# Optimization experiments

Measured on AMD Instinct MI355X. Metric: run time of the kernel, lower is better.

## Reference

```python
import jax, jax.numpy as jnp
import numpy as np

D = 1024; DI = 2048; HS = 16; PS = DI // HS; NS = 64; KC = 4; CHUNK = 64
HA = 16; HKV = 4; PA = D // HA; MLP_MULT = 4; ROPE_BASE = 10000.0
B_SZ = 2; L_SEQ = 2048


def rms_norm(x):
    eps = jnp.asarray(jnp.finfo(x.dtype).eps, x.dtype)
    return x * jax.lax.rsqrt(jnp.mean(jnp.square(x), axis=-1, keepdims=True) + eps)


def silu(x):
    return x * jax.nn.sigmoid(x)


def apply_rope(x, cos, sin):
    half = x.shape[-1] // 2
    x1, x2 = x[..., :half], x[..., half:]
    return jnp.concatenate([x1 * cos + x2 * sin, -x1 * sin + x2 * cos], axis=-1)


def selective_scan(x, A, Bm, Cm, dt, chunk):
    # x: [B,L,H,P], Bm/Cm: [B,L,H,N], A/dt: [H]. L must be a multiple of chunk.
    Bb, L, H, P = x.shape
    N = Bm.shape[-1]
    decay = jnp.exp(A * dt)  # [H]
    nc = L // chunk
    xp = x.reshape(Bb, nc, chunk, H, P).transpose(0, 1, 3, 2, 4)   # [B,nc,H,cs,P]
    Bp = Bm.reshape(Bb, nc, chunk, H, N).transpose(0, 1, 3, 2, 4)  # [B,nc,H,cs,N]
    Cp = Cm.reshape(Bb, nc, chunk, H, N).transpose(0, 1, 3, 2, 4)
    x_dt = xp * dt[None, None, :, None, None]
    idx = jnp.arange(chunk)
    diff = idx[:, None] - idx[None, :]
    # intra-chunk causal decay matrix L_mat: [H,cs,cs]
    Lm = jnp.where(diff >= 0, decay[:, None, None] ** jnp.maximum(diff, 0), 0.0)
    CB = jnp.einsum('bchqn,bchkn->bchqk', Cp, Bp)
    y_diag = jnp.einsum('bchqk,bchkp->bchqp', CB * Lm[None, None], x_dt)
    # per-chunk states
    decay_rev = decay[:, None] ** (chunk - 1 - idx)[None, :]  # [H,cs]
    states = jnp.einsum('bchtn,bchtp->bchnp', Bp * decay_rev[None, None, :, :, None], x_dt)
    # inter-chunk propagation
    ci = jnp.arange(nc)
    shift = ci[:, None] - ci[None, :] - 1
    cdec = decay ** chunk
    M = jnp.where(shift >= 0, cdec[:, None, None] ** jnp.maximum(shift, 0), 0.0)  # [H,nc,nc]
    h_carry = jnp.einsum('hij,bjhnp->bihnp', M, states)
    decay_out = decay[:, None] ** (idx + 1)[None, :]  # [H,cs]
    y_off = jnp.einsum('bchtn,bchnp->bchtp', Cp, h_carry) * decay_out[None, None, :, :, None]
    y = (y_diag + y_off).transpose(0, 1, 3, 2, 4).reshape(Bb, L, H, P)
    return y


def mlp(n, fc_w, proj_w):
    h = jax.nn.relu(n @ fc_w)
    return jnp.square(h) @ proj_w


def setup_inputs() -> dict:
    key = jax.random.key(0)
    ks = jax.random.split(key, 24)
    w = lambda k, shp, s=0.02: jax.random.normal(k, shp, jnp.float32) * s
    dt_init = jax.random.uniform(ks[0], (HS,), jnp.float32, 0.001, 0.1)
    dt_bias = dt_init + jnp.log(-jnp.expm1(-dt_init))  # inverse softplus
    return {
        'x': jax.random.normal(ks[1], (B_SZ, L_SEQ, D), jnp.float32),
        'in_proj_w': w(ks[2], (D, 2 * DI)),
        'conv_w': w(ks[3], (DI, KC), 0.2),
        'conv_b': jnp.zeros((DI,), jnp.float32),
        'B_proj_w': w(ks[4], (D, HS * NS)),
        'C_proj_w': w(ks[5], (D, HS * NS)),
        'dt_bias': dt_bias,
        'A_log': jnp.log(jnp.arange(1, HS + 1, dtype=jnp.float32)),
        'D_param': jnp.ones((HS,), jnp.float32),
        'out_proj_w': w(ks[6], (DI, D)),
        'resid_mix_m': jnp.stack([jnp.ones(D), jnp.zeros(D)]).astype(jnp.float32),
        'mamba_scale': jnp.ones((D,), jnp.float32),
        'm_fc_w': w(ks[7], (D, MLP_MULT * D)),
        'm_proj_w': w(ks[8], (MLP_MULT * D, D)),
        'm_mlp_scale': jnp.ones((D,), jnp.float32),
        'resid_mix_a': jnp.stack([jnp.ones(D), jnp.zeros(D)]).astype(jnp.float32),
        'q_w': w(ks[9], (D, D)),
        'k_w': w(ks[10], (D, HKV * PA)),
        'v_w': w(ks[11], (D, HKV * PA)),
        'o_w': w(ks[12], (D, D)),
        'q_gain': jnp.full((HA,), 1.0, jnp.float32),
        'attn_scale': jnp.ones((D,), jnp.float32),
        'a_fc_w': w(ks[13], (D, MLP_MULT * D)),
        'a_proj_w': w(ks[14], (MLP_MULT * D, D)),
        'a_mlp_scale': jnp.ones((D,), jnp.float32),
    }


def reference(x, in_proj_w, conv_w, conv_b, B_proj_w, C_proj_w, dt_bias, A_log, D_param, out_proj_w, resid_mix_m, mamba_scale, m_fc_w, m_proj_w, m_mlp_scale, resid_mix_a, q_w, k_w, v_w, o_w, q_gain, attn_scale, a_fc_w, a_proj_w, a_mlp_scale):
    Bb, L, _ = x.shape
    x0 = x
    # ---- Mamba block ----
    xm = resid_mix_m[0][None, None] * x + resid_mix_m[1][None, None] * x0
    n = rms_norm(xm)
    vg = n @ in_proj_w
    value, gate = vg[..., :DI], vg[..., DI:]
    v_t = value.transpose(0, 2, 1)  # [B, DI, L]
    v_conv = jax.lax.conv_general_dilated(
        v_t, conv_w[:, None, :], (1,), [(KC - 1, 0)],
        feature_group_count=DI, dimension_numbers=('NCH', 'OIH', 'NCH')) + conv_b[None, :, None]
    value = silu(v_conv).transpose(0, 2, 1).reshape(Bb, L, HS, PS)
    Bm = (xm @ B_proj_w).reshape(Bb, L, HS, NS)  # B/C use pre-norm (mixed) input
    Cm = (xm @ C_proj_w).reshape(Bb, L, HS, NS)
    dt = jax.nn.softplus(dt_bias)
    A = -jnp.exp(A_log)
    y = selective_scan(value, A, Bm, Cm, dt, CHUNK)
    y = y + D_param[None, None, :, None] * value
    y = (y.reshape(Bb, L, DI) * silu(gate)) @ out_proj_w
    xm = xm + mamba_scale[None, None] * y
    xm = xm + m_mlp_scale[None, None] * mlp(rms_norm(xm), m_fc_w, m_proj_w)
    # ---- Attention block ----
    xa = resid_mix_a[0][None, None] * xm + resid_mix_a[1][None, None] * x0
    n = rms_norm(xa)
    q = (n @ q_w).reshape(Bb, L, HA, PA).transpose(0, 2, 1, 3)
    k = (n @ k_w).reshape(Bb, L, HKV, PA).transpose(0, 2, 1, 3)
    v = (n @ v_w).reshape(Bb, L, HKV, PA).transpose(0, 2, 1, 3)
    q = rms_norm(q); k = rms_norm(k)
    inv_freq = 1.0 / (ROPE_BASE ** (jnp.arange(0, PA, 2, dtype=jnp.float32) / PA))
    f = jnp.outer(jnp.arange(L, dtype=jnp.float32), inv_freq)
    cos, sin = jnp.cos(f)[None, None], jnp.sin(f)[None, None]
    q = apply_rope(q, cos, sin) * q_gain[None, :, None, None]
    k = apply_rope(k, cos, sin)
    G = HA // HKV
    k = jnp.repeat(k, G, axis=1); v = jnp.repeat(v, G, axis=1)
    s = jnp.einsum('bhqd,bhkd->bhqk', q, k) / np.float32(np.sqrt(PA))
    mask = jnp.tril(jnp.ones((L, L), bool))
    s = jnp.where(mask[None, None], s, jnp.asarray(-jnp.inf, s.dtype))
    att = jax.nn.softmax(s, axis=-1)
    y = jnp.einsum('bhqk,bhkd->bhqd', att, v).transpose(0, 2, 1, 3).reshape(Bb, L, D)
    xa = xa + attn_scale[None, None] * (y @ o_w)
    xa = xa + a_mlp_scale[None, None] * mlp(rms_norm(xa), a_fc_w, a_proj_w)
    return xa
```

## Files before the change

kernel.cpp:

```cpp
#include <hip/hip_runtime.h>
#include <hip/hip_bf16.h>
#include <math.h>

#define D_ 1024
#define DI_ 2048
#define HS_ 16
#define PS_ 128
#define NS_ 64
#define HA_ 16
#define HKV_ 4
#define PA_ 64
#define B_ 2
#define L_ 2048
#define NT_ 4096
#define NC_ 32
#define RMS_EPS_ 1.1920929e-7f

typedef __attribute__((ext_vector_type(8))) short short8;
typedef __attribute__((ext_vector_type(4))) float f32x4;

#define GLOAD_LDS16(gp, lp)                                                        \
  __builtin_amdgcn_global_load_lds(                                               \
      (const __attribute__((address_space(1))) unsigned int*)(gp),                \
      (__attribute__((address_space(3))) unsigned int*)(lp), 16, 0, 0)

__global__ __launch_bounds__(256) void transpose_cvt(
    const float* __restrict__ W, __hip_bfloat16* __restrict__ Wt, int K, int N, int ldw) {
  __shared__ float t[32][33];
  int n0 = blockIdx.x * 32, k0 = blockIdx.y * 32;
  int tx = threadIdx.x & 31, ty = threadIdx.x >> 5;
#pragma unroll
  for (int i = 0; i < 4; i++)
    t[ty + i * 8][tx] = W[(size_t)(k0 + ty + i * 8) * ldw + n0 + tx];
  __syncthreads();
#pragma unroll
  for (int i = 0; i < 4; i++)
    Wt[(size_t)(n0 + ty + i * 8) * K + k0 + tx] = __float2bfloat16(t[tx][ty + i * 8]);
}

template<int MODE>
__global__ __launch_bounds__(512) void gemm256_k32(
    const unsigned short* __restrict__ A, const unsigned short* __restrict__ Wt,
    __hip_bfloat16* __restrict__ Cb, int N, int K) {
  __shared__ unsigned short As[3][256 * 32];
  __shared__ unsigned short Bs[3][256 * 32];
  int lid = blockIdx.x;
  int x = lid & 7, r = lid >> 3;
  int bm = ((x >> 2) * 8 + (r & 7)) * 256;
  int bn = ((x & 3) * 4 + (r >> 3)) * 256;
  int tid = threadIdx.x;
  int w = tid >> 6, l = tid & 63;
  int wr = w >> 2, wc = w & 3;
  int l15 = l & 15, lg = l >> 4;
  int rr = tid >> 2, ss = tid & 3;

  f32x4 acc[8][4];
#pragma unroll
  for (int i = 0; i < 8; i++)
#pragma unroll
    for (int j = 0; j < 4; j++) acc[i][j] = (f32x4){0.f, 0.f, 0.f, 0.f};

  auto STAGE = [&](int kt, int nb) {
    int k0 = kt * 32;
#pragma unroll
    for (int p = 0; p < 2; p++) {
      int row = p * 128 + rr;
      int kq = ss ^ ((row >> 1) & 3);
      GLOAD_LDS16(A + (size_t)(bm + row) * K + k0 + kq * 8, &As[nb][row * 32 + ss * 8]);
    }
#pragma unroll
    for (int p = 0; p < 2; p++) {
      int row = p * 128 + rr;
      int kq = ss ^ ((row >> 1) & 3);
      GLOAD_LDS16(Wt + (size_t)(bn + row) * K + k0 + kq * 8, &Bs[nb][row * 32 + ss * 8]);
    }
  };

  int KT = K >> 5;
  STAGE(0, 0);
  STAGE(1, 1);
  int buf = 0;
  for (int t = 0; t < KT; ++t) {
    if (t + 1 < KT) {
      asm volatile("s_waitcnt vmcnt(4)" ::: "memory");
    } else {
      asm volatile("s_waitcnt vmcnt(0)" ::: "memory");
    }
    __builtin_amdgcn_s_barrier();
    __builtin_amdgcn_sched_barrier(0);
    if (t + 2 < KT) STAGE(t + 2, (t + 2) % 3);
    short8 bf[4];
#pragma unroll
    for (int j = 0; j < 4; j++) {
      int row = wc * 64 + j * 16 + l15;
      bf[j] = *(const short8*)&Bs[buf][row * 32 + ((lg ^ ((row >> 1) & 3)) << 3)];
    }
#pragma unroll
    for (int i = 0; i < 8; i++) {
      int row = wr * 128 + i * 16 + l15;
      short8 af = *(const short8*)&As[buf][row * 32 + ((lg ^ ((row >> 1) & 3)) << 3)];
#pragma unroll
      for (int j = 0; j < 4; j++)
        acc[i][j] = __builtin_amdgcn_mfma_f32_16x16x32_bf16(af, bf[j], acc[i][j], 0, 0, 0);
    }
    buf = (buf == 2) ? 0 : buf + 1;
  }
#pragma unroll
  for (int i = 0; i < 8; i++)
#pragma unroll
    for (int j = 0; j < 4; j++) {
      int gr = bm + wr * 128 + i * 16 + lg * 4;
      int gc = bn + wc * 64 + j * 16 + l15;
#pragma unroll
      for (int reg = 0; reg < 4; reg++) {
        float v = acc[i][j][reg];
        if (MODE == 1) { v = fmaxf(v, 0.f); v = v * v; }
        Cb[(size_t)(gr + reg) * N + gc] = __float2bfloat16(v);
      }
    }
}

template<int BN>
__global__ __launch_bounds__(256) void gemm_bf16_t(
    const unsigned short* __restrict__ A, const unsigned short* __restrict__ Wt,
    float* __restrict__ Cf, __hip_bfloat16* __restrict__ Cb,
    const float* __restrict__ baseb, const float* __restrict__ scale,
    int N, int K, int gn, int mode, int rsh) {
  constexpr int nWc = BN / 64;
  constexpr int nWr = 4 / nWc;
  constexpr int MF  = 8 / nWr;
  __shared__ unsigned short As[2][128 * 64];
  __shared__ unsigned short Bs[2][BN * 64];
  int lid = blockIdx.x;
  int x = lid & 7, r = lid >> 3;
  int bm, bn;
  if (rsh == 0) {
    int RN = gn >> 2;
    bm = ((x >> 2) * 16 + (r & 15)) * 128;
    bn = ((x & 3) * RN + (r >> 4)) * BN;
  } else {
    bm = (x * 4 + (r & 3)) * 128;
    bn = (r >> 2) * BN;
  }
  int tid = threadIdx.x;
  int w = tid >> 6, l = tid & 63;
  int wr = w / nWc, wc = w % nWc;
  int l15 = l & 15, lg = l >> 4;
  f32x4 acc[MF][4];
#pragma unroll
  for (int i = 0; i < MF; i++)
#pragma unroll
    for (int j = 0; j < 4; j++) acc[i][j] = (f32x4){0.f, 0.f, 0.f, 0.f};
  int r_ = tid >> 3;
  int s_ = tid & 7;

  auto STAGE = [&](int k0, int nb) {
#pragma unroll
    for (int i = 0; i < 4; i++) {
      int rr = i * 32 + r_;
      int kq = s_ ^ (rr & 7);
      GLOAD_LDS16(A + (size_t)(bm + rr) * K + k0 + kq * 8, &As[nb][rr * 64 + s_ * 8]);
    }
#pragma unroll
    for (int i = 0; i < BN / 32; i++) {
      int rr = i * 32 + r_;
      int kq = s_ ^ (rr & 7);
      GLOAD_LDS16(Wt + (size_t)(bn + rr) * K + k0 + kq * 8, &Bs[nb][rr * 64 + s_ * 8]);
    }
  };

  STAGE(0, 0);
  __syncthreads();
  int cur = 0;
  for (int k0 = 0; k0 < K; k0 += 64) {
    if (k0 + 64 < K) STAGE(k0 + 64, cur ^ 1);
#pragma unroll
    for (int h = 0; h < 2; h++) {
      short8 af[MF], bfr[4];
#pragma unroll
      for (int i = 0; i < MF; i++) {
        int row = wr * (16 * MF) + i * 16 + l15;
        int c = h * 4 + lg;
        af[i] = *(const short8*)&As[cur][row * 64 + ((c ^ (row & 7)) << 3)];
      }
#pragma unroll
      for (int j = 0; j < 4; j++) {
        int row = wc * 64 + j * 16 + l15;
        int c = h * 4 + lg;
        bfr[j] = *(const short8*)&Bs[cur][row * 64 + ((c ^ (row & 7)) << 3)];
      }
#pragma unroll
      for (int i = 0; i < MF; i++)
#pragma unroll
        for (int j = 0; j < 4; j++)
          acc[i][j] = __builtin_amdgcn_mfma_f32_16x16x32_bf16(af[i], bfr[j], acc[i][j], 0, 0, 0);
    }
    __syncthreads();
    cur ^= 1;
  }
  int rb = lg * 4, cb2 = l15;
#pragma unroll
  for (int i = 0; i < MF; i++)
#pragma unroll
    for (int j = 0; j < 4; j++) {
      int gr = bm + wr * (16 * MF) + i * 16 + rb;
      int gc = bn + wc * 64 + j * 16 + cb2;
#pragma unroll
      for (int reg = 0; reg < 4; reg++) {
        float v = acc[i][j][reg];
        size_t idx = (size_t)(gr + reg) * N + gc;
        if (mode == 0) {
          Cf[idx] = v;
        } else if (mode == 1) {
          v = fmaxf(v, 0.f);
          Cb[idx] = __float2bfloat16(v * v);
        } else if (mode == 2) {
          Cb[idx] = __float2bfloat16(v);
        } else {
          Cf[idx] = baseb[idx] + scale[gc] * v;
        }
      }
    }
}

__global__ __launch_bounds__(256) void mix_rms_kernel(
    const float* __restrict__ a, const float* __restrict__ b2,
    const float* __restrict__ mix, float* __restrict__ xout,
    __hip_bfloat16* __restrict__ nbf, __hip_bfloat16* __restrict__ rawbf) {
  int row = blockIdx.x;
  size_t base = (size_t)row * D_;
  float v[4]; float ss = 0.f;
#pragma unroll
  for (int i = 0; i < 4; i++) {
    int d = threadIdx.x + i * 256;
    float val = mix[d] * a[base + d] + mix[D_ + d] * b2[base + d];
    v[i] = val; ss += val * val;
  }
  for (int o = 32; o > 0; o >>= 1) ss += __shfl_down(ss, o, 64);
  __shared__ float red[4];
  if ((threadIdx.x & 63) == 0) red[threadIdx.x >> 6] = ss;
  __syncthreads();
  float inv = rsqrtf((red[0] + red[1] + red[2] + red[3]) * (1.f / D_) + RMS_EPS_);
#pragma unroll
  for (int i = 0; i < 4; i++) {
    int d = threadIdx.x + i * 256;
    xout[base + d] = v[i];
    nbf[base + d] = __float2bfloat16(v[i] * inv);
    if (rawbf) rawbf[base + d] = __float2bfloat16(v[i]);
  }
}

__global__ __launch_bounds__(256) void rms_kernel(
    const float* __restrict__ a, __hip_bfloat16* __restrict__ nbf) {
  int row = blockIdx.x;
  size_t base = (size_t)row * D_;
  float v[4]; float ss = 0.f;
#pragma unroll
  for (int i = 0; i < 4; i++) {
    int d = threadIdx.x + i * 256;
    float val = a[base + d];
    v[i] = val; ss += val * val;
  }
  for (int o = 32; o > 0; o >>= 1) ss += __shfl_down(ss, o, 64);
  __shared__ float red[4];
  if ((threadIdx.x & 63) == 0) red[threadIdx.x >> 6] = ss;
  __syncthreads();
  float inv = rsqrtf((red[0] + red[1] + red[2] + red[3]) * (1.f / D_) + RMS_EPS_);
#pragma unroll
  for (int i = 0; i < 4; i++) {
    int d = threadIdx.x + i * 256;
    nbf[base + d] = __float2bfloat16(v[i] * inv);
  }
}

__global__ __launch_bounds__(256) void conv_silu_kernel(
    const __hip_bfloat16* __restrict__ vg, const float* __restrict__ cw,
    const float* __restrict__ cb, float* __restrict__ xv) {
  int idx = blockIdx.x * 256 + threadIdx.x;
  int c = idx & (DI_ - 1);
  int bl = idx >> 11;
  int l = bl & (L_ - 1);
  float acc = cb[c];
  float w0 = cw[c * 4 + 0], w1 = cw[c * 4 + 1], w2 = cw[c * 4 + 2], w3 = cw[c * 4 + 3];
  size_t rb = (size_t)bl * 4096 + c;
  if (l >= 3) acc += __bfloat162float(vg[rb - (size_t)3 * 4096]) * w0;
  if (l >= 2) acc += __bfloat162float(vg[rb - (size_t)2 * 4096]) * w1;
  if (l >= 1) acc += __bfloat162float(vg[rb - (size_t)1 * 4096]) * w2;
  acc += __bfloat162float(vg[rb]) * w3;
  xv[idx] = acc / (1.f + __expf(-acc));
}

__global__ __launch_bounds__(256) void scanA1_kernel(
    const float* __restrict__ xv, const __hip_bfloat16* __restrict__ BCm,
    const float* __restrict__ dt_bias, const float* __restrict__ A_log,
    float* __restrict__ st) {
  __shared__ __align__(16) float sm[4096 + 8192];
  float* Bs = sm;
  float* Xs = sm + 4096;
  int blk = blockIdx.x;
  int c = blk & 31, h = (blk >> 5) & 15, b = blk >> 9;
  float dt = log1pf(__expf(dt_bias[h]));
  float adt = -__expf(A_log[h]) * dt;
  int tid = threadIdx.x;
  int l0 = c * 64;
  size_t rB = ((size_t)(b * L_ + l0)) * 2048 + h * NS_;
#pragma unroll
  for (int i = 0; i < 16; i++) {
    int e = tid + i * 256;
    int t = e >> 6, n = e & 63;
    Bs[t * 64 + n] = __bfloat162float(BCm[rB + (size_t)t * 2048 + n]);
  }
  size_t rX = ((size_t)(b * L_ + l0)) * DI_ + h * PS_;
#pragma unroll
  for (int i = 0; i < 32; i++) {
    int e = tid + i * 256;
    int t = e >> 7, p = e & 127;
    Xs[t * 128 + p] = xv[rX + (size_t)t * DI_ + p];
  }
  __syncthreads();
  int pg = tid & 31;
  int ng = (tid >> 5) << 3;
  float acc[8][4];
#pragma unroll
  for (int nn = 0; nn < 8; nn++)
#pragma unroll
    for (int i = 0; i < 4; i++) acc[nn][i] = 0.f;
  for (int t = 0; t < 64; t++) {
    float dr = __expf(adt * (float)(63 - t));
    float4 x4 = *(const float4*)&Xs[t * 128 + pg * 4];
    float xd0 = x4.x * dr, xd1 = x4.y * dr, xd2 = x4.z * dr, xd3 = x4.w * dr;
#pragma unroll
    for (int nn = 0; nn < 8; nn++) {
      float bv = Bs[t * 64 + ng + nn];
      acc[nn][0] += bv * xd0; acc[nn][1] += bv * xd1;
      acc[nn][2] += bv * xd2; acc[nn][3] += bv * xd3;
    }
  }
  size_t sb = ((size_t)((b * HS_ + h) * NC_ + c)) * (NS_ * PS_);
#pragma unroll
  for (int nn = 0; nn < 8; nn++) {
    *(float4*)&st[sb + (size_t)(ng + nn) * PS_ + pg * 4] =
        make_float4(acc[nn][0] * dt, acc[nn][1] * dt, acc[nn][2] * dt, acc[nn][3] * dt);
  }
}

__global__ __launch_bounds__(256) void scanA2_kernel(
    const float* __restrict__ xv, const __hip_bfloat16* __restrict__ BCm,
    const float* __restrict__ dt_bias,
    const float* __restrict__ A_log, const float* __restrict__ D_param,
    float* __restrict__ y) {
  __shared__ __align__(16) float sm[4160 + 8192];
  float* Cb = sm;
  float* Bs = sm + 4160;
  float* Xs = sm + 4160;
  int blk = blockIdx.x;
  int c = blk & 31, h = (blk >> 5) & 15, b = blk >> 9;
  float dt = log1pf(__expf(dt_bias[h]));
  float adt = -__expf(A_log[h]) * dt;
  float Dp = D_param[h];
  int tid = threadIdx.x;
  int l0 = c * 64;
  size_t rB = ((size_t)(b * L_ + l0)) * 2048 + h * NS_;
#pragma unroll
  for (int i = 0; i < 16; i++) {
    int e = tid + i * 256;
    int t = e >> 6, n = e & 63;
    Bs[t * 64 + n] = __bfloat162float(BCm[rB + (size_t)t * 2048 + n]);
    Cb[t * 65 + n] = __bfloat162float(BCm[rB + 1024 + (size_t)t * 2048 + n]);
  }
  __syncthreads();
  int q = tid >> 2;
  int kb = (tid & 3) << 4;
  float cbl[16];
#pragma unroll
  for (int kk = 0; kk < 16; kk++) {
    int k = kb + kk;
    float a = 0.f;
    if (k <= q) {
      for (int n = 0; n < 64; n++) a += Cb[q * 65 + n] * Bs[k * 64 + n];
      a *= __expf(adt * (float)(q - k));
    }
    cbl[kk] = a;
  }
  __syncthreads();
#pragma unroll
  for (int kk = 0; kk < 16; kk++) Cb[q * 65 + kb + kk] = cbl[kk];
  size_t rX = ((size_t)(b * L_ + l0)) * DI_ + h * PS_;
#pragma unroll
  for (int i = 0; i < 32; i++) {
    int e = tid + i * 256;
    int t = e >> 7, p = e & 127;
    Xs[t * 128 + p] = xv[rX + (size_t)t * DI_ + p];
  }
  __syncthreads();
  int pg = tid & 31;
  int qg = (tid >> 5) << 3;
  float acc[8][4];
#pragma unroll
  for (int qq = 0; qq < 8; qq++)
#pragma unroll
    for (int i = 0; i < 4; i++) acc[qq][i] = 0.f;
  for (int k = 0; k < 64; k++) {
    float4 x4 = *(const float4*)&Xs[k * 128 + pg * 4];
#pragma unroll
    for (int qq = 0; qq < 8; qq++) {
      float s = Cb[(qg + qq) * 65 + k];
      acc[qq][0] += s * x4.x; acc[qq][1] += s * x4.y;
      acc[qq][2] += s * x4.z; acc[qq][3] += s * x4.w;
    }
  }
#pragma unroll
  for (int qq = 0; qq < 8; qq++) {
    int qr = qg + qq;
    float4 xq = *(const float4*)&Xs[qr * 128 + pg * 4];
    size_t yo = ((size_t)(b * L_ + l0 + qr)) * DI_ + h * PS_ + pg * 4;
    *(float4*)&y[yo] = make_float4(acc[qq][0] * dt + Dp * xq.x,
                                   acc[qq][1] * dt + Dp * xq.y,
                                   acc[qq][2] * dt + Dp * xq.z,
                                   acc[qq][3] * dt + Dp * xq.w);
  }
}

__global__ __launch_bounds__(256) void scanB1_kernel(
    float* __restrict__ st, const float* __restrict__ dt_bias,
    const float* __restrict__ A_log) {
  int slice = blockIdx.x & 3;
  int h = (blockIdx.x >> 2) & 15, b = blockIdx.x >> 6;
  float dt = log1pf(__expf(dt_bias[h]));
  float adt = -__expf(A_log[h]) * dt;
  float cdec = __expf(adt * 64.f);
  size_t base = ((size_t)(b * HS_ + h)) * NC_ * (NS_ * PS_) + slice * 2048 + threadIdx.x;
  float hreg[8];
#pragma unroll
  for (int j = 0; j < 8; j++) hreg[j] = 0.f;
  for (int c = 0; c < NC_; c++) {
    size_t o = base + (size_t)c * (NS_ * PS_);
#pragma unroll
    for (int j = 0; j < 8; j++) {
      float tmp = st[o + (size_t)j * 256];
      st[o + (size_t)j * 256] = hreg[j];
      hreg[j] = cdec * hreg[j] + tmp;
    }
  }
}

__global__ __launch_bounds__(256) void scanB2_kernel(
    const __hip_bfloat16* __restrict__ BCm, const float* __restrict__ st,
    const __hip_bfloat16* __restrict__ vg, const float* __restrict__ dt_bias,
    const float* __restrict__ A_log, const float* __restrict__ y,
    __hip_bfloat16* __restrict__ yout) {
  __shared__ float Cs[64 * 64];
  __shared__ __align__(16) float Hs[64 * 128];
  int blk = blockIdx.x;
  int c = blk & 31, h = (blk >> 5) & 15, b = blk >> 9;
  float dt = log1pf(__expf(dt_bias[h]));
  float adt = -__expf(A_log[h]) * dt;
  int tid = threadIdx.x;
  int l0 = c * 64;
  size_t rC = ((size_t)(b * L_ + l0)) * 2048 + 1024 + h * NS_;
#pragma unroll
  for (int i = 0; i < 16; i++) {
    int e = tid + i * 256;
    int t = e >> 6, n = e & 63;
    Cs[t * 64 + n] = __bfloat162float(BCm[rC + (size_t)t * 2048 + n]);
  }
  size_t sb = ((size_t)((b * HS_ + h) * NC_ + c)) * (NS_ * PS_);
#pragma unroll
  for (int i = 0; i < 32; i++) {
    int e = tid + i * 256;
    Hs[e] = st[sb + e];
  }
  __syncthreads();
  int pg = tid & 31;
  int tg = (tid >> 5) << 3;
  float acc[8][4];
#pragma unroll
  for (int tt = 0; tt < 8; tt++)
#pragma unroll
    for (int i = 0; i < 4; i++) acc[tt][i] = 0.f;
  for (int n = 0; n < 64; n++) {
    float4 h4 = *(const float4*)&Hs[n * 128 + pg * 4];
#pragma unroll
    for (int tt = 0; tt < 8; tt++) {
      float cv = Cs[(tg + tt) * 64 + n];
      acc[tt][0] += cv * h4.x; acc[tt][1] += cv * h4.y;
      acc[tt][2] += cv * h4.z; acc[tt][3] += cv * h4.w;
    }
  }
#pragma unroll
  for (int tt = 0; tt < 8; tt++) {
    int t = tg + tt;
    float dout = __expf(adt * (float)(t + 1));
    size_t row = (size_t)(b * L_ + l0 + t);
#pragma unroll
    for (int i = 0; i < 4; i++) {
      int p = pg * 4 + i;
      float g = __bfloat162float(vg[row * 4096 + 2048 + h * PS_ + p]);
      float yv = y[row * DI_ + h * PS_ + p] + acc[tt][i] * dout;
      yout[row * DI_ + h * PS_ + p] = __float2bfloat16(yv * (g / (1.f + __expf(-g))));
    }
  }
}

__global__ void rope_fill_kernel(float* __restrict__ cosb, float* __restrict__ sinb) {
  int idx = blockIdx.x * 256 + threadIdx.x;
  int i = idx & 31, l = idx >> 5;
  float inv = __expf(-(2.0f * (float)i / (float)PA_) * logf(10000.0f));
  float ang = (float)l * inv;
  cosb[idx] = cosf(ang);
  sinb[idx] = sinf(ang);
}

__global__ __launch_bounds__(256) void qknorm_rope_bf16_kernel(
    const float* __restrict__ src, int srcstride, int srcofs,
    __hip_bfloat16* __restrict__ dst, int nh,
    const float* __restrict__ cosb, const float* __restrict__ sinb,
    const float* __restrict__ gain) {
  int row = blockIdx.x * 4 + (threadIdx.x >> 6);
  int lane = threadIdx.x & 63;
  int h = row % nh;
  int tok = row / nh;
  int l = tok & (L_ - 1);
  float v = src[(size_t)tok * srcstride + srcofs + h * 64 + lane];
  float ss = v * v;
  for (int o = 32; o > 0; o >>= 1) ss += __shfl_xor(ss, o, 64);
  v *= rsqrtf(ss * (1.f / PA_) + RMS_EPS_);
  float partner = __shfl_xor(v, 32, 64);
  int i = lane & 31;
  float cth = cosb[l * 32 + i], sth = sinb[l * 32 + i];
  float out = (lane < 32) ? (v * cth + partner * sth) : (v * cth - partner * sth);
  if (gain) out *= gain[h];
  dst[(size_t)tok * (nh * 64) + h * 64 + lane] = __float2bfloat16(out);
}

__global__ __launch_bounds__(256) void attn_mfma_kernel(
    const unsigned short* __restrict__ qb, const unsigned short* __restrict__ kb,
    const unsigned short* __restrict__ vt, const float* __restrict__ qgain,
    __hip_bfloat16* __restrict__ ao) {
  __shared__ unsigned short Ks[64][72];
  __shared__ unsigned short Vs[64][72];
  __shared__ unsigned short Psm[4][16][72];
  int blk = blockIdx.x;
  int qi = blk & 15;
  int h  = (blk >> 4) & 15;
  int b  = blk >> 8;
  int hk = h >> 2;
  int tid = threadIdx.x;
  int w = tid >> 6, l = tid & 63;
  int l15 = l & 15, lg = l >> 4;
  int r0 = tid >> 3, s0 = tid & 7;
  float mstat = 8.0f * fabsf(qgain[h]);
  const unsigned short* kbase = kb + (size_t)b * L_ * (HKV_ * PA_) + hk * PA_ + s0 * 8;
  const unsigned short* vbase = vt + ((size_t)(b * HKV_ + hk) * PA_) * L_ + s0 * 8;

  for (int pass = 0; pass < 2; pass++) {
    int qt = pass ? (31 - qi) : qi;
    int q0 = qt * 64;
    int qw = q0 + w * 16;
    short8 qf[2];
    {
      size_t qrow = ((size_t)(b * L_ + qw + l15)) * (HA_ * PA_) + h * PA_;
      qf[0] = *(const short8*)&qb[qrow + lg * 8];
      qf[1] = *(const short8*)&qb[qrow + 32 + lg * 8];
    }
    f32x4 o_acc[4];
#pragma unroll
    for (int db = 0; db < 4; db++) o_acc[db] = (f32x4){0.f, 0.f, 0.f, 0.f};
    f32x4 lsum = (f32x4){0.f, 0.f, 0.f, 0.f};
    int nkt = qt + 1;
    short8 kr0 = *(const short8*)&kbase[(size_t)r0 * (HKV_ * PA_)];
    short8 kr1 = *(const short8*)&kbase[(size_t)(r0 + 32) * (HKV_ * PA_)];
    short8 vr0 = *(const short8*)&vbase[(size_t)r0 * L_];
    short8 vr1 = *(const short8*)&vbase[(size_t)(r0 + 32) * L_];
    for (int kt = 0; kt < nkt; kt++) {
      int k0 = kt * 64;
      __syncthreads();
      *(short8*)&Ks[r0][s0 * 8] = kr0;
      *(short8*)&Ks[r0 + 32][s0 * 8] = kr1;
      *(short8*)&Vs[r0][s0 * 8] = vr0;
      *(short8*)&Vs[r0 + 32][s0 * 8] = vr1;
      if (kt + 1 < nkt) {
        int k1 = k0 + 64;
        kr0 = *(const short8*)&kbase[(size_t)(k1 + r0) * (HKV_ * PA_)];
        kr1 = *(const short8*)&kbase[(size_t)(k1 + r0 + 32) * (HKV_ * PA_)];
        vr0 = *(const short8*)&vbase[(size_t)r0 * L_ + k1];
        vr1 = *(const short8*)&vbase[(size_t)(r0 + 32) * L_ + k1];
      }
      __syncthreads();
      f32x4 s_acc[4];
#pragma unroll
      for (int kb2 = 0; kb2 < 4; kb2++) {
        short8 b0 = *(const short8*)&Ks[kb2 * 16 + l15][lg * 8];
        short8 b1 = *(const short8*)&Ks[kb2 * 16 + l15][32 + lg * 8];
        f32x4 s = (f32x4){0.f, 0.f, 0.f, 0.f};
        s = __builtin_amdgcn_mfma_f32_16x16x32_bf16(qf[0], b0, s, 0, 0, 0);
        s = __builtin_amdgcn_mfma_f32_16x16x32_bf16(qf[1], b1, s, 0, 0, 0);
        s_acc[kb2] = s;
      }
      bool diag = (kt == qt);
#pragma unroll
      for (int kb2 = 0; kb2 < 4; kb2++) {
        int key = k0 + kb2 * 16 + l15;
#pragma unroll
        for (int reg = 0; reg < 4; reg++) {
          float p = __expf(s_acc[kb2][reg] * 0.125f - mstat);
          if (diag && key > qw + lg * 4 + reg) p = 0.f;
          lsum[reg] += p;
          __hip_bfloat16 hv = __float2bfloat16(p);
          Psm[w][lg * 4 + reg][kb2 * 16 + l15] = *(unsigned short*)&hv;
        }
      }
      asm volatile("s_waitcnt lgkmcnt(0)" ::: "memory");
#pragma unroll
      for (int ks = 0; ks < 2; ks++) {
        short8 pa = *(const short8*)&Psm[w][l15][ks * 32 + lg * 8];
#pragma unroll
        for (int db = 0; db < 4; db++) {
          short8 vb8 = *(const short8*)&Vs[db * 16 + l15][ks * 32 + lg * 8];
          o_acc[db] = __builtin_amdgcn_mfma_f32_16x16x32_bf16(pa, vb8, o_acc[db], 0, 0, 0);
        }
      }
    }
#pragma unroll
    for (int of = 1; of < 16; of <<= 1) {
      lsum[0] += __shfl_xor(lsum[0], of, 64);
      lsum[1] += __shfl_xor(lsum[1], of, 64);
      lsum[2] += __shfl_xor(lsum[2], of, 64);
      lsum[3] += __shfl_xor(lsum[3], of, 64);
    }
#pragma unroll
    for (int reg = 0; reg < 4; reg++) {
      float invl = 1.0f / lsum[reg];
      size_t row = (size_t)(b * L_ + qw + lg * 4 + reg);
#pragma unroll
      for (int db = 0; db < 4; db++)
        ao[row * D_ + h * PA_ + db * 16 + l15] = __float2bfloat16(o_acc[db][reg] * invl);
    }
  }
}

extern "C" void kernel_launch(void* const* d_in, const int* in_sizes, int n_in,
                              void* d_out, int out_size, void* d_ws, size_t ws_size,
                              hipStream_t stream) {
  (void)in_sizes; (void)n_in; (void)out_size; (void)ws_size;
  const float* x           = (const float*)d_in[0];
  const float* in_proj_w   = (const float*)d_in[1];
  const float* conv_w      = (const float*)d_in[2];
  const float* conv_b      = (const float*)d_in[3];
  const float* B_proj_w    = (const float*)d_in[4];
  const float* C_proj_w    = (const float*)d_in[5];
  const float* dt_bias     = (const float*)d_in[6];
  const float* A_log       = (const float*)d_in[7];
  const float* D_param     = (const float*)d_in[8];
  const float* out_proj_w  = (const float*)d_in[9];
  const float* resid_mix_m = (const float*)d_in[10];
  const float* mamba_scale = (const float*)d_in[11];
  const float* m_fc_w      = (const float*)d_in[12];
  const float* m_proj_w    = (const float*)d_in[13];
  const float* m_mlp_scale = (const float*)d_in[14];
  const float* resid_mix_a = (const float*)d_in[15];
  const float* q_w         = (const float*)d_in[16];
  const float* k_w         = (const float*)d_in[17];
  const float* v_w         = (const float*)d_in[18];
  const float* o_w         = (const float*)d_in[19];
  const float* q_gain      = (const float*)d_in[20];
  const float* attn_scale  = (const float*)d_in[21];
  const float* a_fc_w      = (const float*)d_in[22];
  const float* a_proj_w    = (const float*)d_in[23];
  const float* a_mlp_scale = (const float*)d_in[24];
  float* ws  = (float*)d_ws;
  float* out = (float*)d_out;

  float* xm    = ws;
  float* vgR   = ws + 4194304;
  float* xvR   = ws + 12582912;
  float* stR   = ws + 20971520;
  float* nbR   = ws + 29360128;
  float* xmbR  = ws + 31457280;
  float* BCR   = ws + 33554432;
  float* WtR   = ws + 37748736;
  float* cosb  = ws + 51642368;
  float* sinb  = cosb + 65536;

  __hip_bfloat16* vg  = (__hip_bfloat16*)vgR;
  float*          qkvf = vgR;
  float*          xv  = xvR;
  float*          st  = stR;
  __hip_bfloat16* hb  = (__hip_bfloat16*)stR;
  __hip_bfloat16* nbb = (__hip_bfloat16*)nbR;
  __hip_bfloat16* xmb = (__hip_bfloat16*)xmbR;
  __hip_bfloat16* ybb = (__hip_bfloat16*)nbR;
  __hip_bfloat16* BCm = (__hip_bfloat16*)BCR;
  __hip_bfloat16* qbb = (__hip_bfloat16*)xvR;
  __hip_bfloat16* kbb = (__hip_bfloat16*)(xvR + 2097152);
  __hip_bfloat16* vtb = (__hip_bfloat16*)(xvR + 2621440);
  __hip_bfloat16* aob = (__hip_bfloat16*)(xvR + 3145728);

  __hip_bfloat16* Wt = (__hip_bfloat16*)WtR;
  size_t o_in  = 0;
  size_t o_B   = o_in  + (size_t)4096 * 1024;
  size_t o_out = o_B   + (size_t)2048 * 1024;
  size_t o_mfc = o_out + (size_t)1024 * 2048;
  size_t o_mpj = o_mfc + (size_t)4096 * 1024;
  size_t o_qkv = o_mpj + (size_t)1024 * 4096;
  size_t o_o   = o_qkv + (size_t)1536 * 1024;
  size_t o_afc = o_o   + (size_t)1024 * 1024;
  size_t o_apj = o_afc + (size_t)4096 * 1024;

#define TCVT(Wp, off, K, N) \
  transpose_cvt<<<dim3((N) / 32, (K) / 32), 256, 0, stream>>>((Wp), Wt + (off), (K), (N), (N))
  TCVT(in_proj_w,  o_in,  1024, 4096);
  TCVT(B_proj_w,   o_B,   1024, 1024);
  TCVT(C_proj_w,   o_B + (size_t)1024 * 1024, 1024, 1024);
  TCVT(out_proj_w, o_out, 2048, 1024);
  TCVT(m_fc_w,     o_mfc, 1024, 4096);
  TCVT(m_proj_w,   o_mpj, 4096, 1024);
  TCVT(q_w,        o_qkv, 1024, 1024);
  TCVT(k_w,        o_qkv + (size_t)1024 * 1024, 1024, 256);
  TCVT(v_w,        o_qkv + (size_t)1280 * 1024, 1024, 256);
  TCVT(o_w,        o_o,   1024, 1024);
  TCVT(a_fc_w,     o_afc, 1024, 4096);
  TCVT(a_proj_w,   o_apj, 4096, 1024);
#undef TCVT

#define GEMM(BN, Abuf, Woff, Cfp, Cbp, basep, scalep, N, K, mode, rsh) \
  gemm_bf16_t<BN><<<32 * ((N) / (BN)), 256, 0, stream>>>( \
      (const unsigned short*)(Abuf), (const unsigned short*)(Wt + (Woff)), \
      (Cfp), (Cbp), (basep), (scalep), (N), (K), (N) / (BN), (mode), (rsh))
#define GEMM256(MODE, Abuf, Woff, Cbp) \
  gemm256_k32<MODE><<<256, 512, 0, stream>>>( \
      (const unsigned short*)(Abuf), (const unsigned short*)(Wt + (Woff)), \
      (Cbp), 4096, 1024)

  mix_rms_kernel<<<NT_, 256, 0, stream>>>(x, x, resid_mix_m, xm, nbb, xmb);
  GEMM256(2, nbb, o_in, vg);
  GEMM(128, xmb, o_B, (float*)0, BCm, (const float*)0, (const float*)0, 2048, 1024, 2, 0);
  conv_silu_kernel<<<NT_ * DI_ / 256, 256, 0, stream>>>(vg, conv_w, conv_b, xv);
  scanA1_kernel<<<B_ * HS_ * NC_, 256, 0, stream>>>(xv, BCm, dt_bias, A_log, st);
  scanA2_kernel<<<B_ * HS_ * NC_, 256, 0, stream>>>(xv, BCm, dt_bias, A_log, D_param, xv);
  scanB1_kernel<<<B_ * HS_ * 4, 256, 0, stream>>>(st, dt_bias, A_log);
  scanB2_kernel<<<B_ * HS_ * NC_, 256, 0, stream>>>(BCm, st, vg, dt_bias, A_log, xv, ybb);
  GEMM(64, ybb, o_out, xm, (__hip_bfloat16*)0, xm, mamba_scale, 1024, 2048, 3, 1);
  rms_kernel<<<NT_, 256, 0, stream>>>(xm, nbb);
  GEMM256(1, nbb, o_mfc, hb);
  GEMM(64, hb, o_mpj, xm, (__hip_bfloat16*)0, xm, m_mlp_scale, 1024, 4096, 3, 1);
  mix_rms_kernel<<<NT_, 256, 0, stream>>>(xm, x, resid_mix_a, xm, nbb, (__hip_bfloat16*)0);
  GEMM(64, nbb, o_qkv, qkvf, (__hip_bfloat16*)0, (const float*)0, (const float*)0, 1536, 1024, 0, 0);
  rope_fill_kernel<<<L_ * 32 / 256, 256, 0, stream>>>(cosb, sinb);
  qknorm_rope_bf16_kernel<<<NT_ * HA_ / 4, 256, 0, stream>>>(qkvf, 1536, 0, qbb, HA_, cosb, sinb, q_gain);
  qknorm_rope_bf16_kernel<<<NT_ * HKV_ / 4, 256, 0, stream>>>(qkvf, 1536, 1024, kbb, HKV_, cosb, sinb, (const float*)0);
  transpose_cvt<<<dim3(256 / 32, 2048 / 32), 256, 0, stream>>>(qkvf + 1280, vtb, 2048, 256, 1536);
  transpose_cvt<<<dim3(256 / 32, 2048 / 32), 256, 0, stream>>>(qkvf + (size_t)L_ * 1536 + 1280, vtb + (size_t)256 * L_, 2048, 256, 1536);
  attn_mfma_kernel<<<B_ * HA_ * 16, 256, 0, stream>>>(
      (const unsigned short*)qbb, (const unsigned short*)kbb, (const unsigned short*)vtb,
      q_gain, aob);
  GEMM(64, aob, o_o, xm, (__hip_bfloat16*)0, xm, attn_scale, 1024, 1024, 3, 0);
  rms_kernel<<<NT_, 256, 0, stream>>>(xm, nbb);
  GEMM256(1, nbb, o_afc, hb);
  GEMM(64, hb, o_apj, out, (__hip_bfloat16*)0, xm, a_mlp_scale, 1024, 4096, 3, 1);
#undef GEMM
#undef GEMM256
}
```

Before: 687.6 us.

## Add 64x64-tile double-buffered GEMM for narrow-N projections

Adds a new gemm64 kernel that uses 64x64 output tiles, double-buffered LDS staging through direct global-to-LDS loads with an XOR swizzle, and a grouped block-index mapping. It replaces the templated GEMM for the N=1024/1536 projections (out_proj, MLP down-projections, QKV, O). With 4096 rows the smaller tiles launch more blocks, which should fill the CUs better and overlap loads with MFMA work. The cost is less data reuse per block and more redundant reads of A and B.

```diff
diff --git a/kernel.cpp b/kernel.cpp
--- a/kernel.cpp
+++ b/kernel.cpp
@@ -221,6 +221,74 @@
         }
       }
     }
+}
+
+__global__ __launch_bounds__(256) void gemm64(
+    const unsigned short* __restrict__ A, const unsigned short* __restrict__ Wt,
+    float* __restrict__ Cf, const float* __restrict__ baseb,
+    const float* __restrict__ scale, int N, int K, int mode) {
+  __shared__ unsigned short As[2][64 * 64];
+  __shared__ unsigned short Bs[2][64 * 64];
+  int lid = blockIdx.x;
+  int x = lid & 7, r = lid >> 3;
+  int bm = (x * 8 + (r & 7)) * 64;
+  int bn = (r >> 3) * 64;
+  int tid = threadIdx.x;
+  int w = tid >> 6, l = tid & 63;
+  int l15 = l & 15, lg = l >> 4;
+  f32x4 acc[4];
+#pragma unroll
+  for (int j = 0; j < 4; j++) acc[j] = (f32x4){0.f, 0.f, 0.f, 0.f};
+  int r_ = tid >> 3;
+  int s_ = tid & 7;
+
+  auto STAGE = [&](int k0, int nb) {
+#pragma unroll
+    for (int i = 0; i < 2; i++) {
+      int row = i * 32 + r_;
+      int kq = s_ ^ (row & 7);
+      GLOAD_LDS16(A + (size_t)(bm + row) * K + k0 + kq * 8, &As[nb][row * 64 + s_ * 8]);
+    }
+#pragma unroll
+    for (int i = 0; i < 2; i++) {
+      int row = i * 32 + r_;
+      int kq = s_ ^ (row & 7);
+      GLOAD_LDS16(Wt + (size_t)(bn + row) * K + k0 + kq * 8, &Bs[nb][row * 64 + s_ * 8]);
+    }
+  };
+
+  STAGE(0, 0);
+  __syncthreads();
+  int cur = 0;
+  for (int k0 = 0; k0 < K; k0 += 64) {
+    if (k0 + 64 < K) STAGE(k0 + 64, cur ^ 1);
+#pragma unroll
+    for (int h = 0; h < 2; h++) {
+      int c = h * 4 + lg;
+      int arow = w * 16 + l15;
+      short8 af = *(const short8*)&As[cur][arow * 64 + ((c ^ (arow & 7)) << 3)];
+#pragma unroll
+      for (int j = 0; j < 4; j++) {
+        int brow = j * 16 + l15;
+        short8 bfr = *(const short8*)&Bs[cur][brow * 64 + ((c ^ (brow & 7)) << 3)];
+        acc[j] = __builtin_amdgcn_mfma_f32_16x16x32_bf16(af, bfr, acc[j], 0, 0, 0);
+      }
+    }
+    __syncthreads();
+    cur ^= 1;
+  }
+#pragma unroll
+  for (int j = 0; j < 4; j++) {
+    int gr = bm + w * 16 + lg * 4;
+    int gc = bn + j * 16 + l15;
+#pragma unroll
+    for (int reg = 0; reg < 4; reg++) {
+      float v = acc[j][reg];
+      size_t idx = (size_t)(gr + reg) * N + gc;
+      if (mode == 0) Cf[idx] = v;
+      else           Cf[idx] = baseb[idx] + scale[gc] * v;
+    }
+  }
 }
 
 __global__ __launch_bounds__(256) void mix_rms_kernel(
@@ -727,6 +795,10 @@
   gemm_bf16_t<BN><<<32 * ((N) / (BN)), 256, 0, stream>>>( \
       (const unsigned short*)(Abuf), (const unsigned short*)(Wt + (Woff)), \
       (Cfp), (Cbp), (basep), (scalep), (N), (K), (N) / (BN), (mode), (rsh))
+#define GEMM64(Abuf, Woff, Cfp, basep, scalep, N, K, mode) \
+  gemm64<<<64 * ((N) / 64), 256, 0, stream>>>( \
+      (const unsigned short*)(Abuf), (const unsigned short*)(Wt + (Woff)), \
+      (Cfp), (basep), (scalep), (N), (K), (mode))
 #define GEMM256(MODE, Abuf, Woff, Cbp) \
   gemm256_k32<MODE><<<256, 512, 0, stream>>>( \
       (const unsigned short*)(Abuf), (const unsigned short*)(Wt + (Woff)), \
@@ -740,12 +812,12 @@
   scanA2_kernel<<<B_ * HS_ * NC_, 256, 0, stream>>>(xv, BCm, dt_bias, A_log, D_param, xv);
   scanB1_kernel<<<B_ * HS_ * 4, 256, 0, stream>>>(st, dt_bias, A_log);
   scanB2_kernel<<<B_ * HS_ * NC_, 256, 0, stream>>>(BCm, st, vg, dt_bias, A_log, xv, ybb);
-  GEMM(64, ybb, o_out, xm, (__hip_bfloat16*)0, xm, mamba_scale, 1024, 2048, 3, 1);
+  GEMM64(ybb, o_out, xm, xm, mamba_scale, 1024, 2048, 3);
   rms_kernel<<<NT_, 256, 0, stream>>>(xm, nbb);
   GEMM256(1, nbb, o_mfc, hb);
-  GEMM(64, hb, o_mpj, xm, (__hip_bfloat16*)0, xm, m_mlp_scale, 1024, 4096, 3, 1);
+  GEMM64(hb, o_mpj, xm, xm, m_mlp_scale, 1024, 4096, 3);
   mix_rms_kernel<<<NT_, 256, 0, stream>>>(xm, x, resid_mix_a, xm, nbb, (__hip_bfloat16*)0);
-  GEMM(64, nbb, o_qkv, qkvf, (__hip_bfloat16*)0, (const float*)0, (const float*)0, 1536, 1024, 0, 0);
+  GEMM64(nbb, o_qkv, qkvf, (const float*)0, (const float*)0, 1536, 1024, 0);
   rope_fill_kernel<<<L_ * 32 / 256, 256, 0, stream>>>(cosb, sinb);
   qknorm_rope_bf16_kernel<<<NT_ * HA_ / 4, 256, 0, stream>>>(qkvf, 1536, 0, qbb, HA_, cosb, sinb, q_gain);
   qknorm_rope_bf16_kernel<<<NT_ * HKV_ / 4, 256, 0, stream>>>(qkvf, 1536, 1024, kbb, HKV_, cosb, sinb, (const float*)0);
@@ -754,10 +826,11 @@
   attn_mfma_kernel<<<B_ * HA_ * 16, 256, 0, stream>>>(
       (const unsigned short*)qbb, (const unsigned short*)kbb, (const unsigned short*)vtb,
       q_gain, aob);
-  GEMM(64, aob, o_o, xm, (__hip_bfloat16*)0, xm, attn_scale, 1024, 1024, 3, 0);
+  GEMM64(aob, o_o, xm, xm, attn_scale, 1024, 1024, 3);
   rms_kernel<<<NT_, 256, 0, stream>>>(xm, nbb);
   GEMM256(1, nbb, o_afc, hb);
-  GEMM(64, hb, o_apj, out, (__hip_bfloat16*)0, xm, a_mlp_scale, 1024, 4096, 3, 1);
+  GEMM64(hb, o_apj, out, xm, a_mlp_scale, 1024, 4096, 3);
 #undef GEMM
+#undef GEMM64
 #undef GEMM256
 }
```

New measurement: 669.9 us. 1.03x faster.
